# Kernel optimization log

Measured on AMD Instinct MI355X. Metric: run time of the kernel, lower is better.

The kernel has to match this reference:

```python
import jax, jax.numpy as jnp
import numpy as np

B, N, C, H = 16, 577, 768, 12
KEEP_RATE = 0.7


def setup_inputs() -> dict:
    key = jax.random.key(0)
    k1, k2, k3 = jax.random.split(key, 3)
    x = jax.random.normal(k1, (B, N, C), dtype=jnp.float32)
    W_qkv = jax.random.normal(k2, (C, 3 * C), dtype=jnp.float32) * 0.02
    W_proj = jax.random.normal(k3, (C, C), dtype=jnp.float32) * 0.02
    b_proj = jnp.zeros((C,), dtype=jnp.float32)
    return {"x": x, "W_qkv": W_qkv, "W_proj": W_proj, "b_proj": b_proj}


def reference(x, W_qkv, W_proj, b_proj):
    b, n, c = x.shape
    h = H
    dh = c // h
    scale = dh ** (-0.5)

    # qkv projection -> q,k,v each [B,H,N,dh]
    qkv = (x @ W_qkv).reshape(b, n, 3, h, dh)
    qkv = jnp.transpose(qkv, (2, 0, 3, 1, 4))
    q, k, v = qkv[0], qkv[1], qkv[2]

    # full attention scores [B,H,N,N] (materialized, as in the source)
    attn = jnp.einsum('bhnd,bhmd->bhnm', q, k) * scale

    # --- top_pool from row-0 (CLS) scores, attn_method == 'SUM_ABS_1' ---
    # attn[:, :, 0, :] -> [B,H,N]; sum |.| over heads -> [B,N] (== mean over C=1 channel)
    attn_weight = jnp.sum(jnp.abs(attn[:, :, 0, :]), axis=1)  # [B,N]
    # exclude_first=True: drop CLS, topk over remaining N-1, alpha1=1, alpha2=0 (C==1 -> std=0)
    w = attn_weight[:, 1:]                       # [B, N-1]
    keep_num = max(int((n - 1) * KEEP_RATE), 1)  # static
    _, idx = jax.lax.top_k(w, keep_num)          # [B, keep_num]
    idx = jnp.sort(idx, axis=1)
    idx = jnp.concatenate(
        [jnp.zeros((b, 1), dtype=idx.dtype), idx + 1], axis=1)  # prepend CLS index 0
    # expand to [B, keep_num+1, dim] as in torch (pool dim kwarg == self.dim)
    keep_index = jnp.broadcast_to(idx[:, :, None], (b, keep_num + 1, c))

    # standard attention output
    a = jax.nn.softmax(attn, axis=-1)
    out = jnp.einsum('bhnm,bhmd->bhnd', a, v)    # [B,H,N,dh]
    out = jnp.transpose(out, (0, 2, 1, 3)).reshape(b, n, c)
    out = out @ W_proj + b_proj
    return out, keep_index
```

## Files before the change

kernel.cpp:

```cpp
#include <hip/hip_runtime.h>
#include <hip/hip_bf16.h>
#include <stdint.h>

#define B_    16
#define N_    577
#define C_    768
#define H_    12
#define M_    (B_*N_)
#define QKVN  (3*C_)
#define NKEEP 403
#define KROWS (NKEEP+1)
#define VTLD  640
#define PTLD  72

typedef short s16x8 __attribute__((ext_vector_type(8)));
typedef float f32x4 __attribute__((ext_vector_type(4)));

__device__ __forceinline__ unsigned short f2bf(float x){
  unsigned int u = __float_as_uint(x);
  u += 0x7FFF + ((u >> 16) & 1);
  return (unsigned short)(u >> 16);
}

__device__ __forceinline__ void gld_lds16(const void* g, void* l){
  __builtin_amdgcn_global_load_lds(
      (const __attribute__((address_space(1))) unsigned int*)g,
      (__attribute__((address_space(3))) unsigned int*)l, 16, 0, 0);
}

template<int NT, int M9, int MTILES>
__device__ __forceinline__ void tile_map(int L, int& mt, int& nt){
  constexpr int NB = MTILES*NT;
  int x = L & 7, j = L >> 3;
  if(j < M9*NT){
    nt = j/M9; mt = x*M9 + (j - nt*M9);
  } else {
    int offt = 0;
    #pragma unroll
    for(int y=0;y<8;y++) if(y<x) offt += ((NB-1-y)>>3) + 1 - M9*NT;
    int ft = offt + (j - M9*NT);
    mt = 8*M9 + ft/NT;
    nt = ft - (ft/NT)*NT;
  }
}

__global__ void k_cvt_x(const float* __restrict__ x, unsigned short* __restrict__ xb){
  int i = blockIdx.x*256 + threadIdx.x;
  float4 v = ((const float4*)x)[i];
  ushort4 o; o.x=f2bf(v.x); o.y=f2bf(v.y); o.z=f2bf(v.z); o.w=f2bf(v.w);
  ((ushort4*)xb)[i] = o;
}

__global__ void k_transpose_cvt(const float* __restrict__ in, unsigned short* __restrict__ out,
                                int R, int CC){
  __shared__ float tile[64][65];
  int r0 = blockIdx.y*64, c0 = blockIdx.x*64;
  int tx = threadIdx.x & 63, ty = threadIdx.x >> 6;
  #pragma unroll
  for(int i=0;i<16;i++){
    int r = ty + i*4;
    tile[r][tx] = in[(size_t)(r0+r)*CC + c0 + tx];
  }
  __syncthreads();
  #pragma unroll
  for(int i=0;i<16;i++){
    int c = ty + i*4;
    out[(size_t)(c0+c)*R + r0 + tx] = f2bf(tile[tx][c]);
  }
}

template<int LDC_, bool BF16OUT, bool FUSEV, int NT>
__global__ __launch_bounds__(256) void k_gemm_bt(const unsigned short* __restrict__ A,
                          const unsigned short* __restrict__ Bt,
                          void* __restrict__ Cout,
                          const float* __restrict__ bias, int Mdim,
                          unsigned short* __restrict__ vtbuf){
  __shared__ __align__(16) unsigned short As[128*32];
  __shared__ __align__(16) unsigned short Bs[128*32];
  const int t = threadIdx.x;
  const int w = t>>6, l = t&63, lq = l>>4, lr = l&15;
  const int wm = w>>1, wn = w&1;
  int mt, nt; tile_map<NT, 9, 73>(blockIdx.x, mt, nt);
  const int m0 = mt*128, n0 = nt*128;
  int rA0 = m0 + (t>>2);       if(rA0 >= Mdim) rA0 = Mdim-1;
  int rA1 = m0 + ((t+256)>>2); if(rA1 >= Mdim) rA1 = Mdim-1;
  const unsigned short* gA0 = A  + (size_t)rA0*768 + (t&3)*8;
  const unsigned short* gA1 = A  + (size_t)rA1*768 + (t&3)*8;
  const unsigned short* gB0 = Bt + (size_t)(n0 + (t>>2))*768 + (t&3)*8;
  const unsigned short* gB1 = Bt + (size_t)(n0 + ((t+256)>>2))*768 + (t&3)*8;
  unsigned short* lA0 = As + (size_t)w*512;
  unsigned short* lA1 = As + 2048 + (size_t)w*512;
  unsigned short* lB0 = Bs + (size_t)w*512;
  unsigned short* lB1 = Bs + 2048 + (size_t)w*512;
  f32x4 acc[4][4] = {};
  for(int kt=0; kt<24; ++kt){
    const int ko = kt*32;
    __syncthreads();
    gld_lds16(gA0 + ko, lA0); gld_lds16(gA1 + ko, lA1);
    gld_lds16(gB0 + ko, lB0); gld_lds16(gB1 + ko, lB1);
    __syncthreads();
    s16x8 af[4], bfr[4];
    #pragma unroll
    for(int it=0;it<4;it++) af[it]  = *(const s16x8*)&As[(wm*64+it*16+lr)*32 + lq*8];
    #pragma unroll
    for(int jt=0;jt<4;jt++) bfr[jt] = *(const s16x8*)&Bs[(wn*64+jt*16+lr)*32 + lq*8];
    #pragma unroll
    for(int it=0;it<4;it++)
      #pragma unroll
      for(int jt=0;jt<4;jt++)
        acc[it][jt] = __builtin_amdgcn_mfma_f32_16x16x32_bf16(af[it], bfr[jt], acc[it][jt], 0,0,0);
  }
  if(FUSEV && n0 >= 1536){
    #pragma unroll
    for(int it=0;it<4;it++){
      int tok0 = m0 + wm*64 + it*16 + lq*4;
      #pragma unroll
      for(int jt=0;jt<4;jt++){
        int vrow = (n0 - 1536) + wn*64 + jt*16 + lr;
        ushort4 pk; unsigned short* pks = (unsigned short*)&pk;
        #pragma unroll
        for(int r=0;r<4;r++) pks[r] = f2bf(acc[it][jt][r]);
        int b0 = tok0/577, t0 = tok0 - b0*577;
        if(tok0 + 3 < M_ && t0 + 3 < 577){
          *(ushort4*)&vtbuf[(size_t)(b0*768 + vrow)*VTLD + t0] = pk;
        } else {
          #pragma unroll
          for(int r=0;r<4;r++){
            int tg = tok0 + r;
            if(tg < M_){
              int bb = tg/577, tt = tg - bb*577;
              vtbuf[(size_t)(bb*768 + vrow)*VTLD + tt] = pks[r];
            }
          }
        }
      }
    }
  } else {
    #pragma unroll
    for(int it=0;it<4;it++){
      #pragma unroll
      for(int r=0;r<4;r++){
        int row = m0 + wm*64 + it*16 + lq*4 + r;
        if(row < Mdim){
          #pragma unroll
          for(int jt=0;jt<4;jt++){
            int col = n0 + wn*64 + jt*16 + lr;
            float v = acc[it][jt][r];
            if constexpr (BF16OUT)
              ((unsigned short*)Cout)[(size_t)row*LDC_ + col] = f2bf(v);
            else
              ((float*)Cout)[(size_t)row*LDC_ + col] = v + bias[col];
          }
        }
      }
    }
  }
}

__global__ __launch_bounds__(256) void k_gemm_bt64(const unsigned short* __restrict__ A,
                          const unsigned short* __restrict__ Bt,
                          float* __restrict__ Cout,
                          const float* __restrict__ bias, int Mdim){
  __shared__ __align__(16) unsigned short As[64*32];
  __shared__ __align__(16) unsigned short Bs[128*32];
  const int t = threadIdx.x;
  const int w = t>>6, l = t&63, lq = l>>4, lr = l&15;
  const int wm = w>>1, wn = w&1;
  int mt, nt; tile_map<6, 18, 145>(blockIdx.x, mt, nt);
  const int m0 = mt*64, n0 = nt*128;
  int rA0 = m0 + (t>>2);       if(rA0 >= Mdim) rA0 = Mdim-1;
  const unsigned short* gA0 = A  + (size_t)rA0*768 + (t&3)*8;
  const unsigned short* gB0 = Bt + (size_t)(n0 + (t>>2))*768 + (t&3)*8;
  const unsigned short* gB1 = Bt + (size_t)(n0 + ((t+256)>>2))*768 + (t&3)*8;
  unsigned short* lA0 = As + (size_t)w*512;
  unsigned short* lB0 = Bs + (size_t)w*512;
  unsigned short* lB1 = Bs + 2048 + (size_t)w*512;
  f32x4 acc[2][4] = {};
  for(int kt=0; kt<24; ++kt){
    const int ko = kt*32;
    __syncthreads();
    gld_lds16(gA0 + ko, lA0);
    gld_lds16(gB0 + ko, lB0); gld_lds16(gB1 + ko, lB1);
    __syncthreads();
    s16x8 af[2], bfr[4];
    #pragma unroll
    for(int it=0;it<2;it++) af[it]  = *(const s16x8*)&As[(wm*32+it*16+lr)*32 + lq*8];
    #pragma unroll
    for(int jt=0;jt<4;jt++) bfr[jt] = *(const s16x8*)&Bs[(wn*64+jt*16+lr)*32 + lq*8];
    #pragma unroll
    for(int it=0;it<2;it++)
      #pragma unroll
      for(int jt=0;jt<4;jt++)
        acc[it][jt] = __builtin_amdgcn_mfma_f32_16x16x32_bf16(af[it], bfr[jt], acc[it][jt], 0,0,0);
  }
  #pragma unroll
  for(int it=0;it<2;it++){
    #pragma unroll
    for(int r=0;r<4;r++){
      int row = m0 + wm*32 + it*16 + lq*4 + r;
      if(row < Mdim){
        #pragma unroll
        for(int jt=0;jt<4;jt++){
          int col = n0 + wn*64 + jt*16 + lr;
          Cout[(size_t)row*768 + col] = acc[it][jt][r] + bias[col];
        }
      }
    }
  }
}

__global__ __launch_bounds__(256,4) void k_attn(const unsigned short* __restrict__ qkv,
                                                const unsigned short* __restrict__ vtbuf,
                                                unsigned short* __restrict__ aout){
  __shared__ __align__(16) unsigned short Ks[64*64];
  __shared__ __align__(16) unsigned short Vt[64*64];
  __shared__ __align__(16) unsigned short Ptt[128*PTLD];
  __shared__ float Ls[4][2][16][4];
  const int blk = blockIdx.x;
  const int bh = blk % 192, qt = blk / 192;
  const int b = bh / 12, h = bh % 12;
  const int t = threadIdx.x, w = t>>6, l = t&63, lq = l>>4, lr = l&15;
  const size_t base = (size_t)(b*577)*2304 + h*64;
  const int q0 = qt*128;
  s16x8 bq[2][2];
  #pragma unroll
  for(int it=0;it<2;it++){
    int qrow = q0 + w*32 + it*16 + lr; if(qrow > 576) qrow = 576;
    #pragma unroll
    for(int ks=0;ks<2;ks++)
      bq[it][ks] = *(const s16x8*)&qkv[base + (size_t)qrow*2304 + ks*32 + lq*8];
  }
  const int srow = w*8 + (l>>3);
  const int cswz8 = (((l&7) ^ (l>>3)) << 3);
  unsigned short* ldsK = Ks + (size_t)w*512;
  unsigned short* ldsV = Vt + (size_t)w*512;
  const unsigned short* gVbase = vtbuf + (size_t)(bh*64)*VTLD + cswz8;

  f32x4 acc_o[2][4] = {};
  float lsum[2] = {0.f, 0.f};
  const float CEXP = 0.18033688011112043f;

  auto tile_body = [&](int j0, bool edge){
    __syncthreads();
    #pragma unroll
    for(int i=0;i<2;i++){
      int krow = j0 + i*32 + srow; if(krow > 576) krow = 576;
      gld_lds16(qkv + base + 768 + (size_t)krow*2304 + cswz8, ldsK + i*2048);
      gld_lds16(gVbase + (size_t)(i*32 + srow)*VTLD + j0,     ldsV + i*2048);
    }
    __syncthreads();
    f32x4 accs[2][4] = {};
    #pragma unroll
    for(int ks=0;ks<2;ks++){
      s16x8 ak[4];
      #pragma unroll
      for(int jt=0;jt<4;jt++){
        int j = jt*16 + lr;
        ak[jt] = *(const s16x8*)&Ks[j*64 + (((4*ks+lq) ^ (j&7))<<3)];
      }
      #pragma unroll
      for(int it=0;it<2;it++)
        #pragma unroll
        for(int jt=0;jt<4;jt++)
          accs[it][jt] = __builtin_amdgcn_mfma_f32_16x16x32_bf16(ak[jt], bq[it][ks], accs[it][jt], 0,0,0);
    }
    #pragma unroll
    for(int it=0;it<2;it++){
      int qlocal = w*32 + it*16 + lr;
      #pragma unroll
      for(int jt=0;jt<4;jt++){
        ushort4 pk;
        unsigned short* pks = (unsigned short*)&pk;
        #pragma unroll
        for(int r=0;r<4;r++){
          float p = exp2f(accs[it][jt][r] * CEXP);
          if(edge){ if(j0 + jt*16 + lq*4 + r > 576) p = 0.f; }
          lsum[it] += p;
          pks[r] = f2bf(p);
        }
        *(ushort4*)&Ptt[qlocal*PTLD + jt*16 + lq*4] = pk;
      }
    }
    #pragma unroll
    for(int ks=0;ks<2;ks++){
      s16x8 ap[2], bv[4];
      #pragma unroll
      for(int it=0;it<2;it++)
        ap[it] = *(const s16x8*)&Ptt[(w*32+it*16+lr)*PTLD + ks*32 + lq*8];
      #pragma unroll
      for(int dt=0;dt<4;dt++){
        int d = dt*16 + lr;
        bv[dt] = *(const s16x8*)&Vt[d*64 + (((4*ks+lq) ^ (d&7))<<3)];
      }
      #pragma unroll
      for(int it=0;it<2;it++)
        #pragma unroll
        for(int dt=0;dt<4;dt++)
          acc_o[it][dt] = __builtin_amdgcn_mfma_f32_16x16x32_bf16(ap[it], bv[dt], acc_o[it][dt], 0,0,0);
    }
  };
  for(int j0=0; j0<576; j0+=64) tile_body(j0, false);
  tile_body(576, true);

  #pragma unroll
  for(int it=0;it<2;it++) Ls[w][it][lr][lq] = lsum[it];
  #pragma unroll
  for(int it=0;it<2;it++){
    #pragma unroll
    for(int r=0;r<4;r++){
      int n = q0 + w*32 + it*16 + lq*4 + r;
      if(n <= 576){
        int q16 = lq*4 + r;
        float lt = Ls[w][it][q16][0] + Ls[w][it][q16][1] + Ls[w][it][q16][2] + Ls[w][it][q16][3];
        float inv = 1.f / lt;
        #pragma unroll
        for(int dt=0;dt<4;dt++)
          aout[(size_t)(b*577+n)*768 + h*64 + dt*16 + lr] = f2bf(acc_o[it][dt][r]*inv);
      }
    }
  }
}

__global__ void k_qcls(const float* __restrict__ x, const float* __restrict__ Wqkv,
                       float* __restrict__ qcls){
  __shared__ float xs[768];
  __shared__ float part[4][64];
  const int b = blockIdx.y, j0 = blockIdx.x*64;
  const int t = threadIdx.x;
  const float* xr = x + (size_t)b*577*768;
  xs[t] = xr[t]; xs[t+256] = xr[t+256]; xs[t+512] = xr[t+512];
  __syncthreads();
  const int jl = t & 63, cs = t >> 6;
  float acc = 0.f;
  const float* wp = Wqkv + (size_t)(cs*192)*2304 + j0 + jl;
  #pragma unroll 4
  for(int c=0;c<192;c++){ acc += xs[cs*192+c] * wp[0]; wp += 2304; }
  part[cs][jl] = acc;
  __syncthreads();
  if(t < 64) qcls[b*768 + j0 + t] = part[0][t]+part[1][t]+part[2][t]+part[3][t];
}
__global__ void k_u(const float* __restrict__ Wqkv, const float* __restrict__ qcls,
                    float* __restrict__ u){
  int h = blockIdx.x, b = blockIdx.y, c = threadIdx.x;
  const float* qc = qcls + b*768 + h*64;
  const float* wr = Wqkv + (size_t)c*2304 + 768 + h*64;
  float acc = 0.f;
  #pragma unroll
  for(int d=0;d<64;d++) acc += wr[d]*qc[d];
  u[(size_t)(b*12+h)*768 + c] = acc;
}
__global__ void k_attw(const float* __restrict__ x, const float* __restrict__ u,
                       float* __restrict__ attw){
  int blk = blockIdx.x;
  int b = blk/577, m = blk%577;
  int lane = threadIdx.x;
  const float* xr = x + (size_t)(b*577+m)*768;
  const float* ub = u + (size_t)b*12*768;
  float part[12];
  #pragma unroll
  for(int h=0;h<12;h++) part[h]=0.f;
  #pragma unroll
  for(int i=0;i<12;i++){
    float xv = xr[i*64 + lane];
    #pragma unroll
    for(int h=0;h<12;h++) part[h] += xv * ub[h*768 + i*64 + lane];
  }
  float s = 0.f;
  #pragma unroll
  for(int h=0;h<12;h++){
    float v = part[h];
    #pragma unroll
    for(int off=32; off; off>>=1) v += __shfl_xor(v, off);
    s += fabsf(v);
  }
  if(lane==0) attw[b*577 + m] = 0.125f * s;
}
__global__ void k_topk(const float* __restrict__ attw, int* __restrict__ idxbuf){
  __shared__ float sw[576];
  __shared__ int wtot[9];
  int b = blockIdx.x, t = threadIdx.x;
  float wv = attw[b*577 + 1 + t];
  sw[t] = wv;
  __syncthreads();
  int rank = 0;
  for(int j=0;j<576;j++){
    float wj = sw[j];
    rank += (wj > wv) || (wj == wv && j < t);
  }
  bool kept = rank < NKEEP;
  unsigned long long mask = __ballot(kept);
  int wid = t>>6, lane = t&63;
  int pos = __popcll(mask & ((1ull<<lane)-1ull));
  if(lane==0) wtot[wid] = __popcll(mask);
  __syncthreads();
  int off0 = 0;
  for(int q=0;q<wid;q++) off0 += wtot[q];
  if(kept) idxbuf[b*KROWS + 1 + off0 + pos] = t+1;
  if(t==0) idxbuf[b*KROWS] = 0;
}
__global__ void k_fill_keep(const int* __restrict__ idxbuf, float* __restrict__ out2){
  int i4 = blockIdx.x*256 + threadIdx.x;
  float v = (float)idxbuf[i4/192];
  ((float4*)out2)[i4] = make_float4(v,v,v,v);
}

extern "C" void kernel_launch(void* const* d_in, const int* in_sizes, int n_in,
                              void* d_out, int out_size, void* d_ws, size_t ws_size,
                              hipStream_t stream){
  const float* x     = (const float*)d_in[0];
  const float* Wqkv  = (const float*)d_in[1];
  const float* Wproj = (const float*)d_in[2];
  const float* bias  = (const float*)d_in[3];
  float* out  = (float*)d_out;
  float* out2 = out + (size_t)M_*768;

  char* ws = (char*)d_ws;
  size_t off = 0;
  auto alloc = [&](size_t bytes)->void*{ void* p = ws + off; off += (bytes + 255) & ~(size_t)255; return p; };
  unsigned short* xb     = (unsigned short*)alloc((size_t)M_*768*2);
  unsigned short* wqkvT  = (unsigned short*)alloc((size_t)QKVN*768*2);
  unsigned short* wprojT = (unsigned short*)alloc((size_t)768*768*2);
  unsigned short* qkvb   = (unsigned short*)alloc((size_t)M_*QKVN*2);
  unsigned short* aoutb  = (unsigned short*)alloc((size_t)M_*768*2);
  unsigned short* vtbuf  = (unsigned short*)alloc((size_t)192*64*VTLD*2);
  float* qcls   = (float*)alloc((size_t)16*768*4);
  float* u      = (float*)alloc((size_t)16*12*768*4);
  float* attw   = (float*)alloc((size_t)16*577*4);
  int*   idxbuf = (int*)alloc((size_t)16*KROWS*4);

  k_cvt_x<<<6924, 256, 0, stream>>>(x, xb);
  k_transpose_cvt<<<dim3(36,12), 256, 0, stream>>>(Wqkv,  wqkvT, 768, 2304);
  k_transpose_cvt<<<dim3(12,12), 256, 0, stream>>>(Wproj, wprojT, 768, 768);
  k_gemm_bt<QKVN, true, true, 18><<<73*18, 256, 0, stream>>>(xb, wqkvT, qkvb, nullptr, M_, vtbuf);
  k_qcls<<<dim3(12,16), 256, 0, stream>>>(x, Wqkv, qcls);
  k_u<<<dim3(12,16), 768, 0, stream>>>(Wqkv, qcls, u);
  k_attw<<<16*577, 64, 0, stream>>>(x, u, attw);
  k_topk<<<16, 576, 0, stream>>>(attw, idxbuf);
  k_fill_keep<<<(16*KROWS*768/4 + 255)/256, 256, 0, stream>>>(idxbuf, out2);
  k_attn<<<960, 256, 0, stream>>>(qkvb, vtbuf, aoutb);
  k_gemm_bt64<<<145*6, 256, 0, stream>>>(aoutb, wprojT, out, bias, M_);
}
```

Measured before the change: 282.8 us.

## Register-prefetch next K/V tile during attention compute instead of direct LDS loads

Replaces the per-tile global-to-LDS direct loads, which were bracketed by two __syncthreads, with a software pipeline. The next tile's K and V are loaded into registers while the current tile is computed, then written to LDS at the start of the following iteration. Explicit lgkmcnt waits, s_barrier and sched_barrier control the ordering. This is meant to hide global memory latency behind the MFMA work, at the cost of extra VGPRs and an extra register-to-LDS store step.

```diff
diff --git a/kernel.cpp b/kernel.cpp
--- a/kernel.cpp
+++ b/kernel.cpp
@@ -232,23 +232,38 @@
   }
   const int srow = w*8 + (l>>3);
   const int cswz8 = (((l&7) ^ (l>>3)) << 3);
-  unsigned short* ldsK = Ks + (size_t)w*512;
-  unsigned short* ldsV = Vt + (size_t)w*512;
+  unsigned short* ldsK = Ks + w*512 + l*8;
+  unsigned short* ldsV = Vt + w*512 + l*8;
   const unsigned short* gVbase = vtbuf + (size_t)(bh*64)*VTLD + cswz8;
 
   f32x4 acc_o[2][4] = {};
   float lsum[2] = {0.f, 0.f};
   const float CEXP = 0.18033688011112043f;
 
-  auto tile_body = [&](int j0, bool edge){
-    __syncthreads();
-    #pragma unroll
-    for(int i=0;i<2;i++){
-      int krow = j0 + i*32 + srow; if(krow > 576) krow = 576;
-      gld_lds16(qkv + base + 768 + (size_t)krow*2304 + cswz8, ldsK + i*2048);
-      gld_lds16(gVbase + (size_t)(i*32 + srow)*VTLD + j0,     ldsV + i*2048);
-    }
-    __syncthreads();
+  s16x8 kreg0, kreg1, vreg0, vreg1;
+  auto stage_issue = [&](int tt){
+    const int j0i = tt*64;
+    int kr0 = j0i + srow;      if(kr0 > 576) kr0 = 576;
+    int kr1 = j0i + 32 + srow; if(kr1 > 576) kr1 = 576;
+    kreg0 = *(const s16x8*)(qkv + base + 768 + (size_t)kr0*2304 + cswz8);
+    kreg1 = *(const s16x8*)(qkv + base + 768 + (size_t)kr1*2304 + cswz8);
+    vreg0 = *(const s16x8*)(gVbase + (size_t)srow*VTLD + j0i);
+    vreg1 = *(const s16x8*)(gVbase + (size_t)(32 + srow)*VTLD + j0i);
+  };
+
+  stage_issue(0);
+  for(int g=0; g<10; ++g){
+    const int j0 = g*64;
+    const bool edge = (g == 9);
+    *(s16x8*)(ldsK)        = kreg0;
+    *(s16x8*)(ldsK + 2048) = kreg1;
+    *(s16x8*)(ldsV)        = vreg0;
+    *(s16x8*)(ldsV + 2048) = vreg1;
+    asm volatile("s_waitcnt lgkmcnt(0)" ::: "memory");
+    __builtin_amdgcn_s_barrier();
+    __builtin_amdgcn_sched_barrier(0);
+    if(g < 9) stage_issue(g+1);
+
     f32x4 accs[2][4] = {};
     #pragma unroll
     for(int ks=0;ks<2;ks++){
@@ -298,9 +313,10 @@
         for(int dt=0;dt<4;dt++)
           acc_o[it][dt] = __builtin_amdgcn_mfma_f32_16x16x32_bf16(ap[it], bv[dt], acc_o[it][dt], 0,0,0);
     }
-  };
-  for(int j0=0; j0<576; j0+=64) tile_body(j0, false);
-  tile_body(576, true);
+    asm volatile("s_waitcnt lgkmcnt(0)" ::: "memory");
+    __builtin_amdgcn_s_barrier();
+    __builtin_amdgcn_sched_barrier(0);
+  }
 
   #pragma unroll
   for(int it=0;it<2;it++) Ls[w][it][lr][lq] = lsum[it];
```

Result: no change. 281.4 us (-0.5%).
